# Optimization experiments

Measured on AMD Instinct MI355X. Metric: run time of the kernel, lower is better.

## Reference

```python
import jax, jax.numpy as jnp
import numpy as np

N, E, IN, OUT = 50000, 1600000, 64, 64
DIM, K = 2, 5          # pseudo-coordinate dim, kernel size per dim
KP = K ** DIM          # 25 kernel weight matrices
S = 2 ** DIM           # 4 non-zero linear B-spline basis products per edge
# bit pattern per basis product: bits[s, d] in {0,1}
_BITS = np.array([[(s >> d) & 1 for d in range(DIM)] for s in range(S)], dtype=np.int32)
_OFFS = np.array([K ** (DIM - 1 - d) for d in range(DIM)], dtype=np.int32)  # row-major flatten


def setup_inputs() -> dict:
    key = jax.random.key(0)
    ks = jax.random.split(key, 6)
    x = jax.random.normal(ks[0], (N, IN), dtype=jnp.float32)
    edge_index = jax.random.randint(ks[1], (2, E), 0, N)
    pseudo = jax.random.uniform(ks[2], (E, DIM), dtype=jnp.float32)
    bnd = 1.0 / np.sqrt(KP * IN)  # matches uniform(size) init in reset_parameters
    weight = jax.random.uniform(ks[3], (KP, IN, OUT), dtype=jnp.float32, minval=-bnd, maxval=bnd)
    root_weight = jax.random.uniform(ks[4], (IN, OUT), dtype=jnp.float32, minval=-bnd, maxval=bnd)
    bias = jax.random.uniform(ks[5], (OUT,), dtype=jnp.float32, minval=-bnd, maxval=bnd)
    return {"x": x, "edge_index": edge_index, "pseudo": pseudo,
            "weight": weight, "root_weight": root_weight, "bias": bias}


def _basis_and_index(pseudo):
    # open B-spline, degree 1: scale by (K - 1)
    v = pseudo * jnp.asarray(K - 1, pseudo.dtype)          # [E, DIM]
    lo = jnp.floor(v)
    frac = v - lo                                          # [E, DIM]
    lo = lo.astype(jnp.int32)
    bits = jnp.asarray(_BITS)                              # [S, DIM]
    # basis[e, s] = prod_d (frac if bit else 1-frac)
    terms = jnp.where(bits[None].astype(bool), frac[:, None, :], 1.0 - frac[:, None, :])
    basis = jnp.prod(terms, axis=-1)                       # [E, S]
    idx_d = (lo[:, None, :] + bits[None]) % K              # [E, S, DIM]; wrap is harmless (basis=0 there)
    idx = jnp.sum(idx_d * jnp.asarray(_OFFS), axis=-1)     # [E, S] flat weight index in [0, KP)
    return basis, idx


def reference(x, edge_index, pseudo, weight, root_weight, bias):
    row, col = edge_index[0], edge_index[1]                # row = target, col = source
    basis, idx = _basis_and_index(pseudo)                  # [E,S], [E,S]
    x_src = x[col]                                         # [E, IN] gather
    # Accumulate basis-weighted source features per (target node, kernel index),
    # then apply the dense [KP, IN, OUT] weights once (same math, no [E,IN,OUT] blowup).
    acc = jnp.zeros((N * KP, IN), x.dtype)
    for s in range(S):  # S=4, fixed structural loop
        acc = acc + jax.ops.segment_sum(basis[:, s:s + 1] * x_src,
                                        row * KP + idx[:, s], num_segments=N * KP)
    out = jnp.einsum('nki,kio->no', acc.reshape(N, KP, IN), weight)  # [N, OUT]
    deg = jax.ops.segment_sum(jnp.ones((E,), x.dtype), row, num_segments=N)
    out = out / jnp.clip(deg, 1.0)[:, None]                # mean over neighbors (1/N(i))
    return out + x @ root_weight + bias
```

## Files before the change

### kernel.cpp

```cpp
#include <hip/hip_runtime.h>
#include <hip/hip_fp16.h>
#include <hip/hip_bf16.h>


#define NN    50000
#define EE    1600000
#define NPB   16
#define KD    1664
#define ASTB  1672

#define NB    391
#define NSH   4
#define CCAP  1280
#define CSTR  16

#define REC_B 6250
#define XB_B  1563
#define WT_B  104

typedef unsigned short ushort_t;
typedef __attribute__((ext_vector_type(8))) short short8;
typedef __attribute__((ext_vector_type(4))) float f32x4;

static __device__ __forceinline__ ushort_t f2bf(float f) {
  union { float f; unsigned u; } v; v.f = f;
  return (ushort_t)((v.u + 0x7fffu + ((v.u >> 16) & 1u)) >> 16);
}
static __device__ __forceinline__ unsigned pk2bf(float a, float b) {
  __hip_bfloat162 h = __float22bfloat162_rn(make_float2(a, b));
  union { __hip_bfloat162 h; unsigned u; } cv; cv.h = h; return cv.u;
}
union S8 { short8 s; unsigned u[4]; };

__global__ __launch_bounds__(256) void k_prep(
    const int* __restrict__ ei, const float* __restrict__ pseudo,
    int* __restrict__ ccur, uint2* __restrict__ coarse,
    const float* __restrict__ x, ushort_t* __restrict__ xb,
    const float* __restrict__ w, const float* __restrict__ root,
    ushort_t* __restrict__ wt, int useXB) {
  const int b = blockIdx.x;
  const int tid = threadIdx.x;
  if (b < REC_B) {
    int e = b * 256 + tid;
    int row = ei[e], col = ei[EE + e];
    float2 pv = ((const float2*)pseudo)[e];
    float v0 = pv.x * 4.0f, v1 = pv.y * 4.0f;
    unsigned h0 = __half_as_ushort(__float2half(v0));
    unsigned h1 = __half_as_ushort(__float2half(v1));
    int c4 = (row >> 7) * NSH + (tid & (NSH - 1));
    int slot = atomicAdd(&ccur[c4 * CSTR], 1);
    if (slot < CCAP)
      coarse[(size_t)c4 * CCAP + slot] =
          make_uint2((unsigned)col | ((unsigned)(row & 127) << 16), h0 | (h1 << 16));
  } else if (b < REC_B + XB_B) {
    if (!useXB) return;
    int t = (b - REC_B) * 256 + tid;
    if (t < NN * 8) {
      const float4* xp = (const float4*)x + (size_t)t * 2;
      float4 aa = xp[0], bb = xp[1];
      S8 o;
      o.u[0] = pk2bf(aa.x, aa.y); o.u[1] = pk2bf(aa.z, aa.w);
      o.u[2] = pk2bf(bb.x, bb.y); o.u[3] = pk2bf(bb.z, bb.w);
      ((short8*)xb)[t] = o.s;
    }
  } else {
    int t = (b - REC_B - XB_B) * 256 + tid;
    int idx = t * 4;
    if (idx < 64 * KD) {
      int o = idx / KD, k = idx - o * KD;
#pragma unroll
      for (int q = 0; q < 4; ++q) {
        int kk = k + q;
        int kp = kk >> 6, c = kk & 63;
        int fi = 4 * (c & 15) + (c >> 4);
        wt[idx + q] = (kp < 25) ? f2bf(w[(kp * 64 + fi) * 64 + o])
                                : f2bf(root[fi * 64 + o]);
      }
    }
  }
}

__global__ __launch_bounds__(256) void k_sort(
    const int* __restrict__ ccur, const uint2* __restrict__ coarse,
    uint2* __restrict__ recs, uint2* __restrict__ nfo) {
  __shared__ int cnt[128], lpos[128], scn[128], red[256];
  const int c = blockIdx.x, tid = threadIdx.x;
  if (tid < 128) cnt[tid] = 0;
  const int pc = c * NSH;
  int a = 0;
  for (int i = tid; i < pc; i += 256) a += min(ccur[i * CSTR], CCAP);
  red[tid] = a;
  __syncthreads();
  for (int s = 128; s > 0; s >>= 1) { if (tid < s) red[tid] += red[tid + s]; __syncthreads(); }
  const int base = red[0];
  for (int s = 0; s < NSH; ++s) {
    int n = min(ccur[(pc + s) * CSTR], CCAP);
    const uint2* seg = coarse + (size_t)(pc + s) * CCAP;
    for (int i = tid; i < n; i += 256) atomicAdd(&cnt[(seg[i].x >> 16) & 127], 1);
  }
  __syncthreads();
  if (tid < 128) scn[tid] = cnt[tid];
  __syncthreads();
  for (int ofs = 1; ofs < 128; ofs <<= 1) {
    int v = 0;
    if (tid < 128 && tid >= ofs) v = scn[tid - ofs];
    __syncthreads();
    if (tid < 128 && tid >= ofs) scn[tid] += v;
    __syncthreads();
  }
  if (tid < 128) {
    int excl = scn[tid] - cnt[tid];
    lpos[tid] = base + excl;
    int row = c * 128 + tid;
    if (row < NN) nfo[row] = make_uint2((unsigned)(base + excl), (unsigned)cnt[tid]);
  }
  __syncthreads();
  for (int s = 0; s < NSH; ++s) {
    int n = min(ccur[(pc + s) * CSTR], CCAP);
    const uint2* seg = coarse + (size_t)(pc + s) * CCAP;
    for (int i = tid; i < n; i += 256) {
      uint2 r = seg[i];
      int dst = atomicAdd(&lpos[(r.x >> 16) & 127], 1);
      recs[dst] = make_uint2(r.x & 0xFFFFu, r.y);
    }
  }
}

static __device__ __forceinline__ void issue_chunk(
    unsigned wx, unsigned wy, int base, int quad, int m15,
    const ushort_t* __restrict__ xb, unsigned (&pj)[8], uint2 (&g)[8]) {
#pragma unroll
  for (int j = 0; j < 8; ++j) {
    int e = base + quad * 8 + j;
    unsigned cjv = (unsigned)__shfl((int)wx, e);
    pj[j] = (unsigned)__shfl((int)wy, e);
    g[j] = *(const uint2*)(xb + ((size_t)cjv << 6) + (m15 << 2));
  }
}

static __device__ __forceinline__ void compute_chunk(
    const unsigned (&pj)[8], const uint2 (&g)[8],
    float r0f, float c0f, float r1f, float c1f, f32x4 (&acc)[2][4]) {
  S8 aT0, aT1, bT[4];
#pragma unroll
  for (int p = 0; p < 4; ++p) {
    float a0[2], a1[2];
#pragma unroll
    for (int q = 0; q < 2; ++q) {
      unsigned pv = pj[2 * p + q];
      float v0 = __half2float(__ushort_as_half((ushort_t)(pv & 0xFFFFu)));
      float v1 = __half2float(__ushort_as_half((ushort_t)(pv >> 16)));
      a0[q] = fmaxf(0.f, 1.f - fabsf(v0 - r0f)) * fmaxf(0.f, 1.f - fabsf(v1 - c0f));
      a1[q] = fmaxf(0.f, 1.f - fabsf(v0 - r1f)) * fmaxf(0.f, 1.f - fabsf(v1 - c1f));
    }
    aT0.u[p] = pk2bf(a0[0], a0[1]);
    aT1.u[p] = pk2bf(a1[0], a1[1]);
  }
#pragma unroll
  for (int p = 0; p < 4; ++p) {
    bT[0].u[p] = (g[2 * p].x & 0xFFFFu) | (g[2 * p + 1].x << 16);
    bT[1].u[p] = (g[2 * p].x >> 16)     | (g[2 * p + 1].x & 0xFFFF0000u);
    bT[2].u[p] = (g[2 * p].y & 0xFFFFu) | (g[2 * p + 1].y << 16);
    bT[3].u[p] = (g[2 * p].y >> 16)     | (g[2 * p + 1].y & 0xFFFF0000u);
  }
  __builtin_amdgcn_s_setprio(1);
#pragma unroll
  for (int t = 0; t < 4; ++t) {
    acc[0][t] = __builtin_amdgcn_mfma_f32_16x16x32_bf16(aT0.s, bT[t].s, acc[0][t], 0, 0, 0);
    acc[1][t] = __builtin_amdgcn_mfma_f32_16x16x32_bf16(aT1.s, bT[t].s, acc[1][t], 0, 0, 0);
  }
  __builtin_amdgcn_s_setprio(0);
}

template <bool XBF>
static __device__ __forceinline__ void do_chunk(
    const uint2 (&rq)[8], int kb, int m, int quad, int m15,
    float r0f, float c0f, float r1f, float c1f,
    const ushort_t* __restrict__ xb, const float* __restrict__ x,
    f32x4 (&acc)[2][4]) {
  unsigned cj[8], pj[8];
#pragma unroll
  for (int j = 0; j < 8; ++j) {
    cj[j] = min(rq[j].x, (unsigned)(NN - 1));
    pj[j] = rq[j].y;
  }
  uint2 g[8];
  float gf[4][8];
  if (XBF) {
#pragma unroll
    for (int j = 0; j < 8; ++j)
      g[j] = *(const uint2*)(xb + ((size_t)cj[j] << 6) + (m15 << 2));
  } else {
#pragma unroll
    for (int j = 0; j < 8; ++j) {
      float4 v = *(const float4*)(x + ((size_t)cj[j] << 6) + (m15 << 2));
      gf[0][j] = v.x; gf[1][j] = v.y; gf[2][j] = v.z; gf[3][j] = v.w;
    }
  }
  S8 aT0, aT1, bT[4];
#pragma unroll
  for (int p = 0; p < 4; ++p) {
    float a0[2], a1[2];
#pragma unroll
    for (int q = 0; q < 2; ++q) {
      int j = 2 * p + q;
      unsigned pv = pj[j];
      float v0 = __half2float(__ushort_as_half((ushort_t)(pv & 0xFFFFu)));
      float v1 = __half2float(__ushort_as_half((ushort_t)(pv >> 16)));
      bool ok = (kb + quad * 8 + j) < m;
      float p0 = fmaxf(0.f, 1.f - fabsf(v0 - r0f)) * fmaxf(0.f, 1.f - fabsf(v1 - c0f));
      float p1 = fmaxf(0.f, 1.f - fabsf(v0 - r1f)) * fmaxf(0.f, 1.f - fabsf(v1 - c1f));
      a0[q] = ok ? p0 : 0.0f;
      a1[q] = ok ? p1 : 0.0f;
    }
    aT0.u[p] = pk2bf(a0[0], a0[1]);
    aT1.u[p] = pk2bf(a1[0], a1[1]);
  }
  if (XBF) {
#pragma unroll
    for (int p = 0; p < 4; ++p) {
      bT[0].u[p] = (g[2 * p].x & 0xFFFFu) | (g[2 * p + 1].x << 16);
      bT[1].u[p] = (g[2 * p].x >> 16)     | (g[2 * p + 1].x & 0xFFFF0000u);
      bT[2].u[p] = (g[2 * p].y & 0xFFFFu) | (g[2 * p + 1].y << 16);
      bT[3].u[p] = (g[2 * p].y >> 16)     | (g[2 * p + 1].y & 0xFFFF0000u);
    }
  } else {
#pragma unroll
    for (int p = 0; p < 4; ++p)
#pragma unroll
      for (int t = 0; t < 4; ++t)
        bT[t].u[p] = pk2bf(gf[t][2 * p], gf[t][2 * p + 1]);
  }
#pragma unroll
  for (int t = 0; t < 4; ++t) {
    acc[0][t] = __builtin_amdgcn_mfma_f32_16x16x32_bf16(aT0.s, bT[t].s, acc[0][t], 0, 0, 0);
    acc[1][t] = __builtin_amdgcn_mfma_f32_16x16x32_bf16(aT1.s, bT[t].s, acc[1][t], 0, 0, 0);
  }
}

static __device__ __forceinline__ void spill_acc(
    ushort_t* accS, int row, int quad, int m15, const f32x4 (&acc)[2][4]) {
#pragma unroll
  for (int mt = 0; mt < 2; ++mt)
#pragma unroll
    for (int r = 0; r < 4; ++r) {
      int kp = mt * 16 + quad * 4 + r;
      if (kp < 25) {
#pragma unroll
        for (int nt = 0; nt < 4; ++nt)
          accS[row * ASTB + kp * 64 + nt * 16 + m15] = f2bf(acc[mt][nt][r]);
      }
    }
}

template <bool XBF>
__global__ __launch_bounds__(512, 4) void k_main(
    const uint2* __restrict__ recs, const uint2* __restrict__ nfo,
    const float* __restrict__ x, const ushort_t* __restrict__ xb,
    const ushort_t* __restrict__ wt, const float* __restrict__ bias,
    float* __restrict__ out) {
  __shared__ ushort_t accS[NPB * ASTB];
  __shared__ float    outp[2 * NPB * 64];
  __shared__ float    sinv[NPB];
  const int tid = threadIdx.x;
  const int lane = tid & 63;
  const int w = tid >> 6;
  const int nb = blockIdx.x * NPB;

  const int m15 = lane & 15, quad = lane >> 4;
  const float r0f = (float)(m15 / 5),        c0f = (float)(m15 % 5);
  const float r1f = (float)((16 + m15) / 5), c1f = (float)((16 + m15) % 5);
  const int fl = 4 * m15 + quad;

  const int rowA = w << 1, rowB = rowA + 1;
  const int nodeA = nb + rowA, nodeB = nb + rowB;

  const uint2 nfA = nfo[nodeA], nfB = nfo[nodeB];
  const float rxA = x[(size_t)nodeA * 64 + fl];
  const float rxB = x[(size_t)nodeB * 64 + fl];
  const int mA = (int)nfA.y, mB = (int)nfB.y;
  unsigned wAx = 0u, wAy = 0x7C007C00u, wBx = 0u, wBy = 0x7C007C00u;
  if (lane < mA) { uint2 rr = recs[nfA.x + lane]; wAx = rr.x; wAy = rr.y; }
  if (lane < mB) { uint2 rr = recs[nfB.x + lane]; wBx = rr.x; wBy = rr.y; }

  const float dcfA = (float)max(mA, 1), dcfB = (float)max(mB, 1);
  if (lane == 0) { sinv[rowA] = 1.0f / dcfA; sinv[rowB] = 1.0f / dcfB; }
  accS[rowA * ASTB + 1600 + lane] = f2bf(rxA * dcfA);
  accS[rowB * ASTB + 1600 + lane] = f2bf(rxB * dcfB);

  f32x4 acc[2][4];
#pragma unroll
  for (int a = 0; a < 2; ++a)
#pragma unroll
    for (int b = 0; b < 4; ++b) acc[a][b] = (f32x4){0.f, 0.f, 0.f, 0.f};

  if (XBF) {
    if (mA > 32) {
      unsigned pj0[8], pj1[8]; uint2 g0[8], g1[8];
      issue_chunk(wAx, wAy, 0,  quad, m15, xb, pj0, g0);
      issue_chunk(wAx, wAy, 32, quad, m15, xb, pj1, g1);
      compute_chunk(pj0, g0, r0f, c0f, r1f, c1f, acc);
      compute_chunk(pj1, g1, r0f, c0f, r1f, c1f, acc);
    } else if (mA > 0) {
      unsigned pj0[8]; uint2 g0[8];
      issue_chunk(wAx, wAy, 0, quad, m15, xb, pj0, g0);
      compute_chunk(pj0, g0, r0f, c0f, r1f, c1f, acc);
    }
    for (int e0 = 64; e0 < mA; e0 += 32) {
      uint2 rq[8];
#pragma unroll
      for (int j = 0; j < 8; ++j) rq[j] = recs[nfA.x + e0 + quad * 8 + j];
      do_chunk<true>(rq, e0, mA, quad, m15, r0f, c0f, r1f, c1f, xb, x, acc);
    }
    spill_acc(accS, rowA, quad, m15, acc);

#pragma unroll
    for (int a = 0; a < 2; ++a)
#pragma unroll
      for (int b = 0; b < 4; ++b) acc[a][b] = (f32x4){0.f, 0.f, 0.f, 0.f};
    if (mB > 32) {
      unsigned pj0[8], pj1[8]; uint2 g0[8], g1[8];
      issue_chunk(wBx, wBy, 0,  quad, m15, xb, pj0, g0);
      issue_chunk(wBx, wBy, 32, quad, m15, xb, pj1, g1);
      compute_chunk(pj0, g0, r0f, c0f, r1f, c1f, acc);
      compute_chunk(pj1, g1, r0f, c0f, r1f, c1f, acc);
    } else if (mB > 0) {
      unsigned pj0[8]; uint2 g0[8];
      issue_chunk(wBx, wBy, 0, quad, m15, xb, pj0, g0);
      compute_chunk(pj0, g0, r0f, c0f, r1f, c1f, acc);
    }
    for (int e0 = 64; e0 < mB; e0 += 32) {
      uint2 rq[8];
#pragma unroll
      for (int j = 0; j < 8; ++j) rq[j] = recs[nfB.x + e0 + quad * 8 + j];
      do_chunk<true>(rq, e0, mB, quad, m15, r0f, c0f, r1f, c1f, xb, x, acc);
    }
    spill_acc(accS, rowB, quad, m15, acc);
  } else {
    for (int e0 = 0; e0 < mA; e0 += 32) {
      uint2 rq[8];
#pragma unroll
      for (int j = 0; j < 8; ++j) rq[j] = recs[nfA.x + e0 + quad * 8 + j];
      do_chunk<false>(rq, e0, mA, quad, m15, r0f, c0f, r1f, c1f, xb, x, acc);
    }
    spill_acc(accS, rowA, quad, m15, acc);
#pragma unroll
    for (int a = 0; a < 2; ++a)
#pragma unroll
      for (int b = 0; b < 4; ++b) acc[a][b] = (f32x4){0.f, 0.f, 0.f, 0.f};
    for (int e0 = 0; e0 < mB; e0 += 32) {
      uint2 rq[8];
#pragma unroll
      for (int j = 0; j < 8; ++j) rq[j] = recs[nfB.x + e0 + quad * 8 + j];
      do_chunk<false>(rq, e0, mB, quad, m15, r0f, c0f, r1f, c1f, xb, x, acc);
    }
    spill_acc(accS, rowB, quad, m15, acc);
  }
  __syncthreads();

  {
    const int ntile = w & 3, kh = w >> 2;
    const int m2 = lane & 15, quad2 = lane >> 4;
    const int nn2 = ntile * 16 + m2;
    f32x4 d = {0.0f, 0.0f, 0.0f, 0.0f};
    const ushort_t* ab = &accS[m2 * ASTB + kh * 832 + quad2 * 8];
    const ushort_t* wb = &wt[(size_t)nn2 * KD + kh * 832 + quad2 * 8];
    short8 bfs[6];
#pragma unroll
    for (int kk = 0; kk < 6; ++kk) bfs[kk] = *(const short8*)(wb + kk * 32);
#pragma unroll
    for (int kk = 0; kk < 26; ++kk) {
      short8 af = *(const short8*)(ab + kk * 32);
      d = __builtin_amdgcn_mfma_f32_16x16x32_bf16(af, bfs[kk % 6], d, 0, 0, 0);
      if (kk + 6 < 26) bfs[kk % 6] = *(const short8*)(wb + (kk + 6) * 32);
    }
#pragma unroll
    for (int r = 0; r < 4; ++r)
      outp[kh * (NPB * 64) + (quad2 * 4 + r) * 64 + ntile * 16 + m2] = d[r];
  }
  __syncthreads();

  {
#pragma unroll
    for (int h = 0; h < 2; ++h) {
      int i = h * 512 + tid;
      int nl = i >> 6, o = i & 63;
      float conv = outp[i] + outp[NPB * 64 + i];
      out[(size_t)(nb + nl) * 64 + o] = conv * sinv[nl] + bias[o];
    }
  }
}

__global__ void k_sentinel(float* __restrict__ out) {
  int i = blockIdx.x * 256 + threadIdx.x;
  if (i < NN * 64) out[i] = 1000.0f;
}

extern "C" void kernel_launch(void* const* d_in, const int* in_sizes, int n_in,
                              void* d_out, int out_size, void* d_ws, size_t ws_size,
                              hipStream_t stream) {
  const float* x      = (const float*)d_in[0];
  const int*   ei     = (const int*)d_in[1];
  const float* pseudo = (const float*)d_in[2];
  const float* w      = (const float*)d_in[3];
  const float* root   = (const float*)d_in[4];
  const float* bias   = (const float*)d_in[5];
  float* out = (float*)d_out;
  (void)in_sizes; (void)n_in; (void)out_size;

  char* ws = (char*)d_ws;
  size_t off = 0;
  auto alloc = [&](size_t bytes) { size_t r = off; off += (bytes + 511) & ~(size_t)511; return r; };
  ushort_t* wt     = (ushort_t*)(ws + alloc((size_t)64 * KD * 2));
  int*      ccur   = (int*)(ws + alloc((size_t)NB * NSH * CSTR * 4));
  uint2*    nfo    = (uint2*)(ws + alloc((size_t)NN * 8));
  uint2*    recs   = (uint2*)(ws + alloc((size_t)EE * 8));
  uint2*    coarse = (uint2*)(ws + alloc((size_t)NB * NSH * CCAP * 8));
  size_t baseNeed  = off;
  ushort_t* xb     = (ushort_t*)(ws + alloc((size_t)NN * 64 * 2));
  size_t fullNeed  = off;

  if (ws_size < baseNeed) {
    k_sentinel<<<(NN * 64 + 255) / 256, 256, 0, stream>>>(out);
    return;
  }
  const int useXB = (ws_size >= fullNeed) ? 1 : 0;

  hipMemsetAsync(ccur, 0, (size_t)NB * NSH * CSTR * 4, stream);
  k_prep<<<REC_B + XB_B + WT_B, 256, 0, stream>>>(ei, pseudo, ccur, coarse,
                                                  x, xb, w, root, wt, useXB);
  k_sort<<<NB, 256, 0, stream>>>(ccur, coarse, recs, nfo);
  if (useXB)
    k_main<true><<<NN / NPB, 512, 0, stream>>>(recs, nfo, x, xb, wt, bias, out);
  else
    k_main<false><<<NN / NPB, 512, 0, stream>>>(recs, nfo, x, xb, wt, bias, out);
}
```

Before: 303.3 us.

## Replace compacted CSR with fixed 64-slot per-node edge buckets plus overflow list

Measured after the change: 305.0 us. About the same (+0.6%).

```diff
diff --git a/kernel.cpp b/kernel.cpp
--- a/kernel.cpp
+++ b/kernel.cpp
@@ -8,6 +8,7 @@
 #define NPB   16
 #define KD    1664
 #define ASTB  1672
+#define OFCAP 16384
 
 #define NB    391
 #define NSH   4
@@ -19,6 +20,7 @@
 #define WT_B  104
 
 typedef unsigned short ushort_t;
+typedef unsigned long long u64_t;
 typedef __attribute__((ext_vector_type(8))) short short8;
 typedef __attribute__((ext_vector_type(4))) float f32x4;
 
@@ -82,37 +84,29 @@
 
 __global__ __launch_bounds__(256) void k_sort(
     const int* __restrict__ ccur, const uint2* __restrict__ coarse,
-    uint2* __restrict__ recs, uint2* __restrict__ nfo) {
-  __shared__ int cnt[128], lpos[128], scn[128], red[256];
+    uint2* __restrict__ recs2, int* __restrict__ degA,
+    uint4* __restrict__ ofl, int* __restrict__ ofc) {
+  __shared__ int cnt[128], lpos[128];
   const int c = blockIdx.x, tid = threadIdx.x;
   if (tid < 128) cnt[tid] = 0;
+  __syncthreads();
   const int pc = c * NSH;
-  int a = 0;
-  for (int i = tid; i < pc; i += 256) a += min(ccur[i * CSTR], CCAP);
-  red[tid] = a;
-  __syncthreads();
-  for (int s = 128; s > 0; s >>= 1) { if (tid < s) red[tid] += red[tid + s]; __syncthreads(); }
-  const int base = red[0];
   for (int s = 0; s < NSH; ++s) {
     int n = min(ccur[(pc + s) * CSTR], CCAP);
     const uint2* seg = coarse + (size_t)(pc + s) * CCAP;
     for (int i = tid; i < n; i += 256) atomicAdd(&cnt[(seg[i].x >> 16) & 127], 1);
   }
   __syncthreads();
-  if (tid < 128) scn[tid] = cnt[tid];
-  __syncthreads();
-  for (int ofs = 1; ofs < 128; ofs <<= 1) {
-    int v = 0;
-    if (tid < 128 && tid >= ofs) v = scn[tid - ofs];
-    __syncthreads();
-    if (tid < 128 && tid >= ofs) scn[tid] += v;
-    __syncthreads();
-  }
   if (tid < 128) {
-    int excl = scn[tid] - cnt[tid];
-    lpos[tid] = base + excl;
     int row = c * 128 + tid;
-    if (row < NN) nfo[row] = make_uint2((unsigned)(base + excl), (unsigned)cnt[tid]);
+    lpos[tid] = row * 64;
+    if (row < NN) degA[row] = cnt[tid];
+  }
+  for (int i = tid; i < 128 * 64; i += 256) {
+    int r7 = i >> 6, sl = i & 63;
+    int row = c * 128 + r7;
+    if (row < NN && sl >= cnt[r7])
+      recs2[(size_t)row * 64 + sl] = make_uint2(0u, 0x7C007C00u);
   }
   __syncthreads();
   for (int s = 0; s < NSH; ++s) {
@@ -120,34 +114,65 @@
     const uint2* seg = coarse + (size_t)(pc + s) * CCAP;
     for (int i = tid; i < n; i += 256) {
       uint2 r = seg[i];
-      int dst = atomicAdd(&lpos[(r.x >> 16) & 127], 1);
-      recs[dst] = make_uint2(r.x & 0xFFFFu, r.y);
-    }
-  }
-}
-
-static __device__ __forceinline__ void issue_chunk(
-    unsigned wx, unsigned wy, int base, int quad, int m15,
-    const ushort_t* __restrict__ xb, unsigned (&pj)[8], uint2 (&g)[8]) {
+      int r7 = (r.x >> 16) & 127;
+      int dst = atomicAdd(&lpos[r7], 1);
+      int sl = dst - (c * 128 + r7) * 64;
+      if (sl < 64) {
+        recs2[dst] = make_uint2(r.x & 0xFFFFu, r.y);
+      } else {
+        int o = atomicAdd(ofc, 1);
+        if (o < OFCAP) {
+          float v0 = __half2float(__ushort_as_half((ushort_t)(r.y & 0xFFFFu)));
+          float v1 = __half2float(__ushort_as_half((ushort_t)(r.y >> 16)));
+          ofl[o] = make_uint4((unsigned)(c * 128 + r7), r.x & 0xFFFFu,
+                              __float_as_uint(v0), __float_as_uint(v1));
+        }
+      }
+    }
+  }
+}
+
+static __device__ __forceinline__ void issue8(
+    const ushort_t* __restrict__ xb, const unsigned (&vo)[8], u64_t (&g)[8]) {
+  asm volatile(
+      "global_load_dwordx2 %[o0], %[a0], %[sb]\n\t"
+      "global_load_dwordx2 %[o1], %[a1], %[sb]\n\t"
+      "global_load_dwordx2 %[o2], %[a2], %[sb]\n\t"
+      "global_load_dwordx2 %[o3], %[a3], %[sb]\n\t"
+      "global_load_dwordx2 %[o4], %[a4], %[sb]\n\t"
+      "global_load_dwordx2 %[o5], %[a5], %[sb]\n\t"
+      "global_load_dwordx2 %[o6], %[a6], %[sb]\n\t"
+      "global_load_dwordx2 %[o7], %[a7], %[sb]\n\t"
+      : [o0] "=&v"(g[0]), [o1] "=&v"(g[1]), [o2] "=&v"(g[2]), [o3] "=&v"(g[3]),
+        [o4] "=&v"(g[4]), [o5] "=&v"(g[5]), [o6] "=&v"(g[6]), [o7] "=&v"(g[7])
+      : [a0] "v"(vo[0]), [a1] "v"(vo[1]), [a2] "v"(vo[2]), [a3] "v"(vo[3]),
+        [a4] "v"(vo[4]), [a5] "v"(vo[5]), [a6] "v"(vo[6]), [a7] "v"(vo[7]),
+        [sb] "s"(xb));
+}
+static __device__ __forceinline__ void wait8(u64_t (&g)[8]) {
+  asm volatile("s_waitcnt vmcnt(0)"
+               : "+v"(g[0]), "+v"(g[1]), "+v"(g[2]), "+v"(g[3]),
+                 "+v"(g[4]), "+v"(g[5]), "+v"(g[6]), "+v"(g[7]));
+}
+
+static __device__ __forceinline__ void vo8(
+    unsigned wx, int base, int quad, int m15, unsigned (&vo)[8]) {
 #pragma unroll
   for (int j = 0; j < 8; ++j) {
-    int e = base + quad * 8 + j;
-    unsigned cjv = (unsigned)__shfl((int)wx, e);
-    pj[j] = (unsigned)__shfl((int)wy, e);
-    g[j] = *(const uint2*)(xb + ((size_t)cjv << 6) + (m15 << 2));
-  }
-}
-
-static __device__ __forceinline__ void compute_chunk(
-    const unsigned (&pj)[8], const uint2 (&g)[8],
-    float r0f, float c0f, float r1f, float c1f, f32x4 (&acc)[2][4]) {
-  S8 aT0, aT1, bT[4];
+    unsigned c = (unsigned)__shfl((int)wx, base + quad * 8 + j);
+    vo[j] = (c << 7) + (unsigned)(m15 << 3);
+  }
+}
+
+static __device__ __forceinline__ void hats8(
+    unsigned wy, int base, int quad, int m15,
+    float r0f, float c0f, float r1f, float c1f, S8& aT0, S8& aT1) {
 #pragma unroll
   for (int p = 0; p < 4; ++p) {
     float a0[2], a1[2];
 #pragma unroll
     for (int q = 0; q < 2; ++q) {
-      unsigned pv = pj[2 * p + q];
+      unsigned pv = (unsigned)__shfl((int)wy, base + quad * 8 + 2 * p + q);
       float v0 = __half2float(__ushort_as_half((ushort_t)(pv & 0xFFFFu)));
       float v1 = __half2float(__ushort_as_half((ushort_t)(pv >> 16)));
       a0[q] = fmaxf(0.f, 1.f - fabsf(v0 - r0f)) * fmaxf(0.f, 1.f - fabsf(v1 - c0f));
@@ -156,12 +181,19 @@
     aT0.u[p] = pk2bf(a0[0], a0[1]);
     aT1.u[p] = pk2bf(a1[0], a1[1]);
   }
+}
+
+static __device__ __forceinline__ void packmfma(
+    const u64_t (&g)[8], const S8& aT0, const S8& aT1, f32x4 (&acc)[2][4]) {
+  S8 bT[4];
 #pragma unroll
   for (int p = 0; p < 4; ++p) {
-    bT[0].u[p] = (g[2 * p].x & 0xFFFFu) | (g[2 * p + 1].x << 16);
-    bT[1].u[p] = (g[2 * p].x >> 16)     | (g[2 * p + 1].x & 0xFFFF0000u);
-    bT[2].u[p] = (g[2 * p].y & 0xFFFFu) | (g[2 * p + 1].y << 16);
-    bT[3].u[p] = (g[2 * p].y >> 16)     | (g[2 * p + 1].y & 0xFFFF0000u);
+    unsigned lo0 = (unsigned)g[2 * p],     hi0 = (unsigned)(g[2 * p] >> 32);
+    unsigned lo1 = (unsigned)g[2 * p + 1], hi1 = (unsigned)(g[2 * p + 1] >> 32);
+    bT[0].u[p] = (lo0 & 0xFFFFu) | (lo1 << 16);
+    bT[1].u[p] = (lo0 >> 16)     | (lo1 & 0xFFFF0000u);
+    bT[2].u[p] = (hi0 & 0xFFFFu) | (hi1 << 16);
+    bT[3].u[p] = (hi0 >> 16)     | (hi1 & 0xFFFF0000u);
   }
   __builtin_amdgcn_s_setprio(1);
 #pragma unroll
@@ -172,30 +204,84 @@
   __builtin_amdgcn_s_setprio(0);
 }
 
-template <bool XBF>
-static __device__ __forceinline__ void do_chunk(
+static __device__ __forceinline__ void node_bf16(
+    unsigned wx, unsigned wy, int m, int quad, int m15,
+    float r0f, float c0f, float r1f, float c1f,
+    const ushort_t* __restrict__ xb, f32x4 (&acc)[2][4]) {
+  if (m > 32) {
+    unsigned vo0[8], vo1[8];
+    u64_t g0[8], g1[8];
+    vo8(wx, 0, quad, m15, vo0);
+    issue8(xb, vo0, g0);
+    vo8(wx, 32, quad, m15, vo1);
+    issue8(xb, vo1, g1);
+    S8 aT0_0, aT1_0, aT0_1, aT1_1;
+    hats8(wy, 0,  quad, m15, r0f, c0f, r1f, c1f, aT0_0, aT1_0);
+    hats8(wy, 32, quad, m15, r0f, c0f, r1f, c1f, aT0_1, aT1_1);
+    __builtin_amdgcn_sched_barrier(0);
+    wait8(g0); wait8(g1);
+    packmfma(g0, aT0_0, aT1_0, acc);
+    packmfma(g1, aT0_1, aT1_1, acc);
+  } else {
+    unsigned vo0[8];
+    u64_t g0[8];
+    vo8(wx, 0, quad, m15, vo0);
+    issue8(xb, vo0, g0);
+    S8 aT0, aT1;
+    hats8(wy, 0, quad, m15, r0f, c0f, r1f, c1f, aT0, aT1);
+    __builtin_amdgcn_sched_barrier(0);
+    wait8(g0);
+    packmfma(g0, aT0, aT1, acc);
+  }
+}
+
+static __device__ __forceinline__ void replay_ofl(
+    const uint4* __restrict__ ofl, int ofcv, int node, int quad, int m15,
+    float r0f, float c0f, float r1f, float c1f,
+    const float* __restrict__ x, f32x4 (&acc)[2][4]) {
+  for (int i = 0; i < ofcv; ++i) {
+    uint4 r = ofl[i];
+    if ((int)r.x != node) continue;
+    float v0 = __uint_as_float(r.z), v1 = __uint_as_float(r.w);
+    float h00 = fmaxf(0.f, 1.f - fabsf(v0 - r0f));
+    float h01 = fmaxf(0.f, 1.f - fabsf(v1 - c0f));
+    float h10 = fmaxf(0.f, 1.f - fabsf(v0 - r1f));
+    float h11 = fmaxf(0.f, 1.f - fabsf(v1 - c1f));
+    float mk = (quad == 0) ? 1.0f : 0.0f;
+    S8 aT0, aT1, bT[4];
+#pragma unroll
+    for (int p = 0; p < 4; ++p) { aT0.u[p] = 0; aT1.u[p] = 0; }
+    aT0.u[0] = pk2bf(h00 * h01 * mk, 0.0f);
+    aT1.u[0] = pk2bf(h10 * h11 * mk, 0.0f);
+    float4 xv = *(const float4*)(x + (size_t)r.y * 64 + (m15 << 2));
+    float fv[4] = {xv.x, xv.y, xv.z, xv.w};
+#pragma unroll
+    for (int t = 0; t < 4; ++t)
+#pragma unroll
+      for (int p = 0; p < 4; ++p) bT[t].u[p] = pk2bf(fv[t], fv[t]);
+#pragma unroll
+    for (int t = 0; t < 4; ++t) {
+      acc[0][t] = __builtin_amdgcn_mfma_f32_16x16x32_bf16(aT0.s, bT[t].s, acc[0][t], 0, 0, 0);
+      acc[1][t] = __builtin_amdgcn_mfma_f32_16x16x32_bf16(aT1.s, bT[t].s, acc[1][t], 0, 0, 0);
+    }
+  }
+}
+
+static __device__ __forceinline__ void do_chunk_f32(
     const uint2 (&rq)[8], int kb, int m, int quad, int m15,
     float r0f, float c0f, float r1f, float c1f,
-    const ushort_t* __restrict__ xb, const float* __restrict__ x,
-    f32x4 (&acc)[2][4]) {
+    const float* __restrict__ x, f32x4 (&acc)[2][4]) {
   unsigned cj[8], pj[8];
 #pragma unroll
   for (int j = 0; j < 8; ++j) {
     cj[j] = min(rq[j].x, (unsigned)(NN - 1));
     pj[j] = rq[j].y;
   }
-  uint2 g[8];
   float gf[4][8];
-  if (XBF) {
-#pragma unroll
-    for (int j = 0; j < 8; ++j)
-      g[j] = *(const uint2*)(xb + ((size_t)cj[j] << 6) + (m15 << 2));
-  } else {
-#pragma unroll
-    for (int j = 0; j < 8; ++j) {
-      float4 v = *(const float4*)(x + ((size_t)cj[j] << 6) + (m15 << 2));
-      gf[0][j] = v.x; gf[1][j] = v.y; gf[2][j] = v.z; gf[3][j] = v.w;
-    }
+#pragma unroll
+  for (int j = 0; j < 8; ++j) {
+    float4 v = *(const float4*)(x + ((size_t)cj[j] << 6) + (m15 << 2));
+    gf[0][j] = v.x; gf[1][j] = v.y; gf[2][j] = v.z; gf[3][j] = v.w;
   }
   S8 aT0, aT1, bT[4];
 #pragma unroll
@@ -216,21 +302,11 @@
     aT0.u[p] = pk2bf(a0[0], a0[1]);
     aT1.u[p] = pk2bf(a1[0], a1[1]);
   }
-  if (XBF) {
-#pragma unroll
-    for (int p = 0; p < 4; ++p) {
-      bT[0].u[p] = (g[2 * p].x & 0xFFFFu) | (g[2 * p + 1].x << 16);
-      bT[1].u[p] = (g[2 * p].x >> 16)     | (g[2 * p + 1].x & 0xFFFF0000u);
-      bT[2].u[p] = (g[2 * p].y & 0xFFFFu) | (g[2 * p + 1].y << 16);
-      bT[3].u[p] = (g[2 * p].y >> 16)     | (g[2 * p + 1].y & 0xFFFF0000u);
-    }
-  } else {
-#pragma unroll
-    for (int p = 0; p < 4; ++p)
-#pragma unroll
-      for (int t = 0; t < 4; ++t)
-        bT[t].u[p] = pk2bf(gf[t][2 * p], gf[t][2 * p + 1]);
-  }
+#pragma unroll
+  for (int p = 0; p < 4; ++p)
+#pragma unroll
+    for (int t = 0; t < 4; ++t)
+      bT[t].u[p] = pk2bf(gf[t][2 * p], gf[t][2 * p + 1]);
 #pragma unroll
   for (int t = 0; t < 4; ++t) {
     acc[0][t] = __builtin_amdgcn_mfma_f32_16x16x32_bf16(aT0.s, bT[t].s, acc[0][t], 0, 0, 0);
@@ -255,7 +331,8 @@
 
 template <bool XBF>
 __global__ __launch_bounds__(512, 4) void k_main(
-    const uint2* __restrict__ recs, const uint2* __restrict__ nfo,
+    const uint2* __restrict__ recs2, const int* __restrict__ degA,
+    const uint4* __restrict__ ofl, const int* __restrict__ ofc,
     const float* __restrict__ x, const ushort_t* __restrict__ xb,
     const ushort_t* __restrict__ wt, const float* __restrict__ bias,
     float* __restrict__ out) {
@@ -275,13 +352,12 @@
   const int rowA = w << 1, rowB = rowA + 1;
   const int nodeA = nb + rowA, nodeB = nb + rowB;
 
-  const uint2 nfA = nfo[nodeA], nfB = nfo[nodeB];
+  const int mA = degA[nodeA], mB = degA[nodeB];
+  uint2 wA = recs2[(size_t)nodeA * 64 + lane];
+  uint2 wB = recs2[(size_t)nodeB * 64 + lane];
   const float rxA = x[(size_t)nodeA * 64 + fl];
   const float rxB = x[(size_t)nodeB * 64 + fl];
-  const int mA = (int)nfA.y, mB = (int)nfB.y;
-  unsigned wAx = 0u, wAy = 0x7C007C00u, wBx = 0u, wBy = 0x7C007C00u;
-  if (lane < mA) { uint2 rr = recs[nfA.x + lane]; wAx = rr.x; wAy = rr.y; }
-  if (lane < mB) { uint2 rr = recs[nfB.x + lane]; wBx = rr.x; wBy = rr.y; }
+  const int ofcv = min(ofc[0], OFCAP);
 
   const float dcfA = (float)max(mA, 1), dcfB = (float)max(mB, 1);
   if (lane == 0) { sinv[rowA] = 1.0f / dcfA; sinv[rowB] = 1.0f / dcfB; }
@@ -295,65 +371,36 @@
     for (int b = 0; b < 4; ++b) acc[a][b] = (f32x4){0.f, 0.f, 0.f, 0.f};
 
   if (XBF) {
-    if (mA > 32) {
-      unsigned pj0[8], pj1[8]; uint2 g0[8], g1[8];
-      issue_chunk(wAx, wAy, 0,  quad, m15, xb, pj0, g0);
-      issue_chunk(wAx, wAy, 32, quad, m15, xb, pj1, g1);
-      compute_chunk(pj0, g0, r0f, c0f, r1f, c1f, acc);
-      compute_chunk(pj1, g1, r0f, c0f, r1f, c1f, acc);
-    } else if (mA > 0) {
-      unsigned pj0[8]; uint2 g0[8];
-      issue_chunk(wAx, wAy, 0, quad, m15, xb, pj0, g0);
-      compute_chunk(pj0, g0, r0f, c0f, r1f, c1f, acc);
-    }
-    for (int e0 = 64; e0 < mA; e0 += 32) {
-      uint2 rq[8];
-#pragma unroll
-      for (int j = 0; j < 8; ++j) rq[j] = recs[nfA.x + e0 + quad * 8 + j];
-      do_chunk<true>(rq, e0, mA, quad, m15, r0f, c0f, r1f, c1f, xb, x, acc);
-    }
+    node_bf16(wA.x, wA.y, mA, quad, m15, r0f, c0f, r1f, c1f, xb, acc);
+    if (ofcv) replay_ofl(ofl, ofcv, nodeA, quad, m15, r0f, c0f, r1f, c1f, x, acc);
     spill_acc(accS, rowA, quad, m15, acc);
-
 #pragma unroll
     for (int a = 0; a < 2; ++a)
 #pragma unroll
       for (int b = 0; b < 4; ++b) acc[a][b] = (f32x4){0.f, 0.f, 0.f, 0.f};
-    if (mB > 32) {
-      unsigned pj0[8], pj1[8]; uint2 g0[8], g1[8];
-      issue_chunk(wBx, wBy, 0,  quad, m15, xb, pj0, g0);
-      issue_chunk(wBx, wBy, 32, quad, m15, xb, pj1, g1);
-      compute_chunk(pj0, g0, r0f, c0f, r1f, c1f, acc);
-      compute_chunk(pj1, g1, r0f, c0f, r1f, c1f, acc);
-    } else if (mB > 0) {
-      unsigned pj0[8]; uint2 g0[8];
-      issue_chunk(wBx, wBy, 0, quad, m15, xb, pj0, g0);
-      compute_chunk(pj0, g0, r0f, c0f, r1f, c1f, acc);
-    }
-    for (int e0 = 64; e0 < mB; e0 += 32) {
-      uint2 rq[8];
-#pragma unroll
-      for (int j = 0; j < 8; ++j) rq[j] = recs[nfB.x + e0 + quad * 8 + j];
-      do_chunk<true>(rq, e0, mB, quad, m15, r0f, c0f, r1f, c1f, xb, x, acc);
-    }
+    node_bf16(wB.x, wB.y, mB, quad, m15, r0f, c0f, r1f, c1f, xb, acc);
+    if (ofcv) replay_ofl(ofl, ofcv, nodeB, quad, m15, r0f, c0f, r1f, c1f, x, acc);
     spill_acc(accS, rowB, quad, m15, acc);
   } else {
-    for (int e0 = 0; e0 < mA; e0 += 32) {
+    for (int e0 = 0; e0 < min(mA, 64); e0 += 32) {
       uint2 rq[8];
 #pragma unroll
-      for (int j = 0; j < 8; ++j) rq[j] = recs[nfA.x + e0 + quad * 8 + j];
-      do_chunk<false>(rq, e0, mA, quad, m15, r0f, c0f, r1f, c1f, xb, x, acc);
-    }
+      for (int j = 0; j < 8; ++j) rq[j] = recs2[(size_t)nodeA * 64 + e0 + quad * 8 + j];
+      do_chunk_f32(rq, e0, mA, quad, m15, r0f, c0f, r1f, c1f, x, acc);
+    }
+    if (ofcv) replay_ofl(ofl, ofcv, nodeA, quad, m15, r0f, c0f, r1f, c1f, x, acc);
     spill_acc(accS, rowA, quad, m15, acc);
 #pragma unroll
     for (int a = 0; a < 2; ++a)
 #pragma unroll
       for (int b = 0; b < 4; ++b) acc[a][b] = (f32x4){0.f, 0.f, 0.f, 0.f};
-    for (int e0 = 0; e0 < mB; e0 += 32) {
+    for (int e0 = 0; e0 < min(mB, 64); e0 += 32) {
       uint2 rq[8];
 #pragma unroll
-      for (int j = 0; j < 8; ++j) rq[j] = recs[nfB.x + e0 + quad * 8 + j];
-      do_chunk<false>(rq, e0, mB, quad, m15, r0f, c0f, r1f, c1f, xb, x, acc);
-    }
+      for (int j = 0; j < 8; ++j) rq[j] = recs2[(size_t)nodeB * 64 + e0 + quad * 8 + j];
+      do_chunk_f32(rq, e0, mB, quad, m15, r0f, c0f, r1f, c1f, x, acc);
+    }
+    if (ofcv) replay_ofl(ofl, ofcv, nodeB, quad, m15, r0f, c0f, r1f, c1f, x, acc);
     spill_acc(accS, rowB, quad, m15, acc);
   }
   __syncthreads();
@@ -412,9 +459,11 @@
   size_t off = 0;
   auto alloc = [&](size_t bytes) { size_t r = off; off += (bytes + 511) & ~(size_t)511; return r; };
   ushort_t* wt     = (ushort_t*)(ws + alloc((size_t)64 * KD * 2));
-  int*      ccur   = (int*)(ws + alloc((size_t)NB * NSH * CSTR * 4));
-  uint2*    nfo    = (uint2*)(ws + alloc((size_t)NN * 8));
-  uint2*    recs   = (uint2*)(ws + alloc((size_t)EE * 8));
+  int*      ccur   = (int*)(ws + alloc((size_t)(NB * NSH * CSTR + 16) * 4));
+  int*      ofcp   = ccur + NB * NSH * CSTR;
+  int*      degA   = (int*)(ws + alloc((size_t)NN * 4));
+  uint4*    ofl    = (uint4*)(ws + alloc((size_t)OFCAP * 16));
+  uint2*    recs2  = (uint2*)(ws + alloc((size_t)NN * 64 * 8));
   uint2*    coarse = (uint2*)(ws + alloc((size_t)NB * NSH * CCAP * 8));
   size_t baseNeed  = off;
   ushort_t* xb     = (ushort_t*)(ws + alloc((size_t)NN * 64 * 2));
@@ -426,12 +475,12 @@
   }
   const int useXB = (ws_size >= fullNeed) ? 1 : 0;
 
-  hipMemsetAsync(ccur, 0, (size_t)NB * NSH * CSTR * 4, stream);
+  hipMemsetAsync(ccur, 0, (size_t)(NB * NSH * CSTR + 16) * 4, stream);
   k_prep<<<REC_B + XB_B + WT_B, 256, 0, stream>>>(ei, pseudo, ccur, coarse,
                                                   x, xb, w, root, wt, useXB);
-  k_sort<<<NB, 256, 0, stream>>>(ccur, coarse, recs, nfo);
+  k_sort<<<NB, 256, 0, stream>>>(ccur, coarse, recs2, degA, ofl, ofcp);
   if (useXB)
-    k_main<true><<<NN / NPB, 512, 0, stream>>>(recs, nfo, x, xb, wt, bias, out);
+    k_main<true><<<NN / NPB, 512, 0, stream>>>(recs2, degA, ofl, ofcp, x, xb, wt, bias, out);
   else
-    k_main<false><<<NN / NPB, 512, 0, stream>>>(recs, nfo, x, xb, wt, bias, out);
-}
+    k_main<false><<<NN / NPB, 512, 0, stream>>>(recs2, degA, ofl, ofcp, x, xb, wt, bias, out);
+}
```
